# Performance work log

Measured on AMD Instinct MI355X. Metric: run time of the kernel, lower is better.

The kernel has to match this reference:

```python
import jax, jax.numpy as jnp
import numpy as np

B, S = 2, 2048
HID = 2048
NH = 16
QLR, KVLR = 1536, 512
DN, DR, DV = 128, 64, 128
QHD = DN + DR  # 192
SCALE = 1.0 / np.sqrt(QHD)
ROPE_BASE = 10000.0


def rope_cos_sin(seq_len, dim):
    inv_freq = 1.0 / (ROPE_BASE ** (jnp.arange(0, dim, 2, dtype=jnp.float32) / dim))
    freqs = jnp.arange(seq_len, dtype=jnp.float32)[:, None] * inv_freq[None, :]  # [S, dim/2]
    emb = jnp.concatenate([freqs, freqs], axis=-1)  # [S, dim]
    return jnp.cos(emb), jnp.sin(emb)


def rotate_half(x):
    h = x.shape[-1] // 2
    return jnp.concatenate([-x[..., h:], x[..., :h]], axis=-1)


def apply_rope(x, cos, sin):
    # x: [B, S, H, D]; cos/sin: [S, D] broadcast per position
    c = cos[None, :, None, :]
    s = sin[None, :, None, :]
    return x * c + rotate_half(x) * s


def setup_inputs() -> dict:
    key = jax.random.key(0)
    ks = jax.random.split(key, 10)
    w = lambda k, shape: (jax.random.normal(k, shape, dtype=jnp.float32) * 0.02)
    causal = jnp.tril(jnp.ones((S, S), dtype=bool))[None, None]  # [1,1,S,S]
    return {
        "hidden_states": jax.random.normal(ks[0], (B, S, HID), dtype=jnp.float32),
        "causal_mask": causal,
        "w_q_a": w(ks[1], (HID, QLR)),
        "w_q_nope": w(ks[2], (QLR, NH * DN)),
        "w_q_rope": w(ks[3], (QLR, NH * DR)),
        "w_kv_a": w(ks[4], (HID, KVLR)),
        "w_k_nope": w(ks[5], (KVLR, NH * DN)),
        "w_k_rope": w(ks[6], (KVLR, NH * DR)),
        "w_v": w(ks[7], (KVLR, NH * DV)),
        "w_o": w(ks[8], (NH * DV, HID)),
    }


def reference(hidden_states, causal_mask, w_q_a, w_q_nope, w_q_rope,
              w_kv_a, w_k_nope, w_k_rope, w_v, w_o):
    b, s, _ = hidden_states.shape
    # LoRA-A compression
    q_c = hidden_states @ w_q_a      # [B,S,QLR]
    kv_c = hidden_states @ w_kv_a    # [B,S,KVLR]
    # LoRA-B expansions (split NOPE / ROPE)
    q_nope = (q_c @ w_q_nope).reshape(b, s, NH, DN)
    q_rope = (q_c @ w_q_rope).reshape(b, s, NH, DR)
    k_nope = (kv_c @ w_k_nope).reshape(b, s, NH, DN)
    k_rope = (kv_c @ w_k_rope).reshape(b, s, NH, DR)
    v = (kv_c @ w_v).reshape(b, s, NH, DV)
    # RoPE on the rope slices only
    cos, sin = rope_cos_sin(s, DR)
    q_rope = apply_rope(q_rope, cos, sin)
    k_rope = apply_rope(k_rope, cos, sin)
    q = jnp.concatenate([q_nope, q_rope], axis=-1)  # [B,S,H,192]
    k = jnp.concatenate([k_nope, k_rope], axis=-1)
    # attention
    scores = jnp.einsum('bqhd,bkhd->bhqk', q, k) * SCALE
    mask_add = jnp.where(causal_mask, 0.0, -10000.0)
    attn = jax.nn.softmax(scores + mask_add, axis=-1)
    out = jnp.einsum('bhqk,bkhd->bqhd', attn, v).reshape(b, s, NH * DV)
    return out @ w_o  # [B,S,HID]
```

## Files before the change

kernel.cpp:

```cpp
#include <hip/hip_runtime.h>
#include <hip/hip_bf16.h>
#include <stdint.h>

typedef __hip_bfloat16 bf16;
typedef __attribute__((ext_vector_type(8))) short bf16x8;
typedef __attribute__((ext_vector_type(4))) float f32x4;

#define MFMA16(a,b,c) __builtin_amdgcn_mfma_f32_16x16x32_bf16((a),(b),(c),0,0,0)

#define BATCH 2
#define S_LEN 2048
#define HID_D 2048
#define NHEAD 16
#define QLR_D 1536
#define KVLR_D 512
#define DN_D 128
#define DR_D 64
#define DV_D 128
#define QKD 192
#define ATT_SCALE 0.07216878364870322f

__device__ __forceinline__ void async_load16(const bf16* g, bf16* l) {
    __builtin_amdgcn_global_load_lds((const __attribute__((address_space(1))) uint32_t*)g,
                                     (__attribute__((address_space(3))) uint32_t*)l,
                                     16, 0, 0);
}

__device__ __forceinline__ unsigned short f2bf_bits(float f) {
    bf16 h = __float2bfloat16(f);
    return *reinterpret_cast<unsigned short*>(&h);
}

template <int CTRL>
__device__ __forceinline__ float dpp_mov(float x) {
    return __builtin_bit_cast(float,
        __builtin_amdgcn_update_dpp(0, __builtin_bit_cast(int, x), CTRL, 0xF, 0xF, true));
}
__device__ __forceinline__ float row_max16(float x) {
    x = fmaxf(x, dpp_mov<0xB1>(x));
    x = fmaxf(x, dpp_mov<0x4E>(x));
    x = fmaxf(x, dpp_mov<0x124>(x));
    x = fmaxf(x, dpp_mov<0x128>(x));
    return x;
}
__device__ __forceinline__ float row_sum16(float x) {
    x += dpp_mov<0xB1>(x);
    x += dpp_mov<0x4E>(x);
    x += dpp_mov<0x124>(x);
    x += dpp_mov<0x128>(x);
    return x;
}

__global__ void convert_bf16_kernel(const float* __restrict__ in, bf16* __restrict__ out, int n) {
    int idx = blockIdx.x * blockDim.x + threadIdx.x;
    int i4 = idx * 4;
    if (i4 >= n) return;
    float4 v = *(const float4*)(in + i4);
    ushort4 o;
    o.x = f2bf_bits(v.x);
    o.y = f2bf_bits(v.y);
    o.z = f2bf_bits(v.z);
    o.w = f2bf_bits(v.w);
    *(ushort4*)(out + i4) = o;
}

__global__ void transpose_convert_kernel(const float* __restrict__ in, bf16* __restrict__ out,
                                         int K, int N) {
    __shared__ float tile[32][33];
    int tx = threadIdx.x;
    int ty = threadIdx.y;
    int n0 = blockIdx.x * 32, k0 = blockIdx.y * 32;
#pragma unroll
    for (int i = 0; i < 4; i++)
        tile[ty + i * 8][tx] = in[(size_t)(k0 + ty + i * 8) * N + n0 + tx];
    __syncthreads();
#pragma unroll
    for (int i = 0; i < 4; i++)
        out[(size_t)(n0 + ty + i * 8) * K + k0 + tx] = __float2bfloat16(tile[tx][ty + i * 8]);
}

template <int MODE>
__global__ __launch_bounds__(256, 2)
void gemm_bt_kernel(const bf16* __restrict__ A, const bf16* __restrict__ Bt,
                    void* __restrict__ C, void* __restrict__ C2,
                    int M, int N, int K, int lda) {
    __shared__ __align__(16) bf16 As[128 * 64];
    __shared__ __align__(16) bf16 Bs[128 * 64];
    const int tid = threadIdx.x;
    const int wave = tid >> 6, lane = tid & 63;
    const int quad = lane >> 4, l16 = lane & 15;
    const int wm = (wave >> 1) * 64, wn = (wave & 1) * 64;
    const int m0 = blockIdx.y * 128, n0 = blockIdx.x * 128;

    f32x4 acc[4][4];
#pragma unroll
    for (int i = 0; i < 4; i++)
#pragma unroll
        for (int j = 0; j < 4; j++)
            acc[i][j] = (f32x4){0.f, 0.f, 0.f, 0.f};

    const bf16* ga = A + (size_t)m0 * lda;
    const bf16* gb = Bt + (size_t)n0 * K;

    for (int k0 = 0; k0 < K; k0 += 64) {
        __syncthreads();
#pragma unroll
        for (int i = 0; i < 4; i++) {
            int chunk = i * 256 + tid;
            int row = chunk >> 3, cseg = chunk & 7;
            int wbase = i * 256 + wave * 64;
            async_load16(ga + (size_t)row * lda + k0 + cseg * 8, &As[wbase * 8]);
            async_load16(gb + (size_t)row * K + k0 + cseg * 8, &Bs[wbase * 8]);
        }
        __syncthreads();
#pragma unroll
        for (int kk = 0; kk < 64; kk += 32) {
            bf16x8 af[4], bfr[4];
#pragma unroll
            for (int t = 0; t < 4; t++) {
                af[t]  = *(const bf16x8*)&As[(wm + t * 16 + l16) * 64 + kk + quad * 8];
                bfr[t] = *(const bf16x8*)&Bs[(wn + t * 16 + l16) * 64 + kk + quad * 8];
            }
#pragma unroll
            for (int tm = 0; tm < 4; tm++)
#pragma unroll
                for (int tn = 0; tn < 4; tn++)
                    acc[tm][tn] = MFMA16(af[tm], bfr[tn], acc[tm][tn]);
        }
    }
#pragma unroll
    for (int tm = 0; tm < 4; tm++)
#pragma unroll
        for (int tn = 0; tn < 4; tn++) {
            const int col = n0 + wn + tn * 16 + l16;
            const int row0 = m0 + wm + tm * 16 + quad * 4;
            if constexpr (MODE == 4) {
                if (n0 >= 3072) {
                    ushort4 pk;
                    pk.x = f2bf_bits(acc[tm][tn][0]);
                    pk.y = f2bf_bits(acc[tm][tn][1]);
                    pk.z = f2bf_bits(acc[tm][tn][2]);
                    pk.w = f2bf_bits(acc[tm][tn][3]);
                    *(ushort4*)((bf16*)C2 + (size_t)(col - 3072) * M + row0) = pk;
                    continue;
                }
            }
#pragma unroll
            for (int r = 0; r < 4; r++) {
                const int row = row0 + r;
                const float v = acc[tm][tn][r];
                if constexpr (MODE == 0)
                    ((bf16*)C)[(size_t)row * N + col] = __float2bfloat16(v);
                else if constexpr (MODE == 1)
                    ((float*)C)[(size_t)row * N + col] = v;
                else if constexpr (MODE == 2) {
                    if (n0 < 2048) {
                        int hh = col >> 7, dd = col & 127;
                        ((bf16*)C)[(size_t)row * (NHEAD * QKD) + hh * QKD + dd] =
                            __float2bfloat16(v);
                    } else {
                        int c2 = col - 2048, hh = c2 >> 6, dd = c2 & 63;
                        ((bf16*)C)[(size_t)row * (NHEAD * QKD) + hh * QKD + 128 + dd] =
                            __float2bfloat16(v);
                    }
                } else {
                    if (n0 < 2048) {
                        int hh = col >> 7, dd = col & 127;
                        ((bf16*)C)[(size_t)row * (NHEAD * QKD) + hh * QKD + dd] =
                            __float2bfloat16(v);
                    } else {
                        int c2 = col - 2048, hh = c2 >> 6, dd = c2 & 63;
                        ((bf16*)C)[(size_t)row * (NHEAD * QKD) + hh * QKD + 128 + dd] =
                            __float2bfloat16(v);
                    }
                }
            }
        }
}

__global__ void rope_kernel(bf16* __restrict__ buf, int nrows) {
    int idx = blockIdx.x * blockDim.x + threadIdx.x;
    if (idx >= nrows * NHEAD * 32) return;
    int j = idx & 31;
    int h = (idx >> 5) & (NHEAD - 1);
    int row = idx >> 9;
    int pos = row & (S_LEN - 1);
    float inv = __expf(-(float)j * (9.210340371976184f / 32.f));
    float f = (float)pos * inv;
    float c = __cosf(f), s = __sinf(f);
    bf16* p = buf + (size_t)row * (NHEAD * QKD) + h * QKD + 128 + j;
    float x1 = __bfloat162float(p[0]);
    float x2 = __bfloat162float(p[32]);
    p[0]  = __float2bfloat16(x1 * c - x2 * s);
    p[32] = __float2bfloat16(x2 * c + x1 * s);
}

__global__ __launch_bounds__(256, 2)
void attn_kernel(const bf16* __restrict__ qf_g, const bf16* __restrict__ kf_g,
                 const bf16* __restrict__ vT, bf16* __restrict__ o_out) {
    __shared__ __align__(16) bf16 k_s[64 * QKD];
    __shared__ __align__(16) bf16 vt_s[128 * 64];
    __shared__ __align__(16) bf16 p_s[4 * 32 * 64];

    const int tid = threadIdx.x;
    const int wave = tid >> 6, lane = tid & 63;
    const int quad = lane >> 4, l16 = lane & 15;
    const int bh = blockIdx.y;
    const int qt = (bh < 16) ? (gridDim.x - 1 - blockIdx.x) : blockIdx.x;
    const int q0 = qt * 128;
    const int b = bh >> 4, h = bh & 15;
    const int tokbase = b * S_LEN;
    const int M = BATCH * S_LEN;

    const int wq = q0 + wave * 32;
    bf16x8 qfr[2][6];
#pragma unroll
    for (int mt = 0; mt < 2; mt++) {
        const bf16* qrow = qf_g + (size_t)(tokbase + wq + mt * 16 + l16) * (NHEAD * QKD)
                                + h * QKD + quad * 8;
#pragma unroll
        for (int kk = 0; kk < 6; kk++)
            qfr[mt][kk] = *(const bf16x8*)(qrow + kk * 32);
    }

    float m_run[2][4], l_run[2][4];
#pragma unroll
    for (int mt = 0; mt < 2; mt++)
#pragma unroll
        for (int r = 0; r < 4; r++) { m_run[mt][r] = -1e30f; l_run[mt][r] = 0.f; }
    f32x4 oacc[2][8];
#pragma unroll
    for (int mt = 0; mt < 2; mt++)
#pragma unroll
        for (int d = 0; d < 8; d++) oacc[mt][d] = (f32x4){0.f, 0.f, 0.f, 0.f};

    const int niter = q0 / 64 + 2;
    for (int it = 0; it < niter; it++) {
        const int kv0 = it * 64;
        __syncthreads();
#pragma unroll
        for (int i = 0; i < 6; i++) {
            int c = i * 256 + tid;
            int row = c / 24, seg = c % 24;
            async_load16(kf_g + (size_t)(tokbase + kv0 + row) * (NHEAD * QKD) + h * QKD + seg * 8,
                         &k_s[(i * 256 + wave * 64) * 8]);
        }
#pragma unroll
        for (int i = 0; i < 4; i++) {
            int c = i * 256 + tid;
            int d = c >> 3, seg = c & 7;
            async_load16(vT + (size_t)(h * 128 + d) * M + tokbase + kv0 + seg * 8,
                         &vt_s[(i * 256 + wave * 64) * 8]);
        }
        __syncthreads();

        if (kv0 <= wq + 31) {
            const bool do0 = kv0 <= wq + 15;
            f32x4 sa[2][4];
#pragma unroll
            for (int mt = 0; mt < 2; mt++)
#pragma unroll
                for (int nt = 0; nt < 4; nt++) sa[mt][nt] = (f32x4){0.f, 0.f, 0.f, 0.f};
#pragma unroll
            for (int kk = 0; kk < 6; kk++) {
                bf16x8 bk[4];
#pragma unroll
                for (int nt = 0; nt < 4; nt++)
                    bk[nt] = *(const bf16x8*)&k_s[(nt * 16 + l16) * QKD + kk * 32 + quad * 8];
#pragma unroll
                for (int mt = 0; mt < 2; mt++)
#pragma unroll
                    for (int nt = 0; nt < 4; nt++)
                        sa[mt][nt] = MFMA16(qfr[mt][kk], bk[nt], sa[mt][nt]);
            }

            auto softmax_mt = [&](int mt) {
                const int qmin = wq + mt * 16;
                const bool needMask = (kv0 + 63) > qmin;
                float alpha[4];
#pragma unroll
                for (int r = 0; r < 4; r++) {
                    const int qpos = qmin + quad * 4 + r;
                    float mx = m_run[mt][r];
                    float sv[4];
#pragma unroll
                    for (int nt = 0; nt < 4; nt++) {
                        float x = sa[mt][nt][r];
                        if (needMask && (kv0 + nt * 16 + l16 > qpos)) x = -1e30f;
                        sv[nt] = x;
                        mx = fmaxf(mx, x);
                    }
                    mx = row_max16(mx);
                    float rs = 0.f;
#pragma unroll
                    for (int nt = 0; nt < 4; nt++) {
                        float p = __expf(ATT_SCALE * (sv[nt] - mx));
                        sv[nt] = p;
                        rs += p;
                    }
                    rs = row_sum16(rs);
                    alpha[r] = __expf(ATT_SCALE * (m_run[mt][r] - mx));
                    l_run[mt][r] = alpha[r] * l_run[mt][r] + rs;
                    m_run[mt][r] = mx;
                    const int row = mt * 16 + quad * 4 + r;
#pragma unroll
                    for (int nt = 0; nt < 4; nt++)
                        p_s[wave * 2048 + row * 64 + ((nt ^ quad) << 4) + l16] =
                            __float2bfloat16(sv[nt]);
                }
#pragma unroll
                for (int d = 0; d < 8; d++)
#pragma unroll
                    for (int r = 0; r < 4; r++) oacc[mt][d][r] *= alpha[r];
            };
            if (do0) softmax_mt(0);
            softmax_mt(1);

#pragma unroll
            for (int kk = 0; kk < 2; kk++) {
                bf16x8 bv[8];
#pragma unroll
                for (int d = 0; d < 8; d++)
                    bv[d] = *(const bf16x8*)&vt_s[(d * 16 + l16) * 64 + kk * 32 + quad * 8];
                const int grp = (kk * 2 + (quad >> 1)) ^ (l16 >> 2);
                const int lo8 = (quad & 1) * 8;
                bf16x8 ap1 = *(const bf16x8*)&p_s[wave * 2048 + (16 + l16) * 64 + (grp << 4) + lo8];
                if (do0) {
                    bf16x8 ap0 = *(const bf16x8*)&p_s[wave * 2048 + l16 * 64 + (grp << 4) + lo8];
#pragma unroll
                    for (int d = 0; d < 8; d++) oacc[0][d] = MFMA16(ap0, bv[d], oacc[0][d]);
                }
#pragma unroll
                for (int d = 0; d < 8; d++) oacc[1][d] = MFMA16(ap1, bv[d], oacc[1][d]);
            }
        }
    }

#pragma unroll
    for (int mt = 0; mt < 2; mt++)
#pragma unroll
        for (int d = 0; d < 8; d++)
#pragma unroll
            for (int r = 0; r < 4; r++) {
                int qrow = wq + mt * 16 + quad * 4 + r;
                int col = h * DV_D + d * 16 + l16;
                o_out[(size_t)(tokbase + qrow) * (NHEAD * DV_D) + col] =
                    __float2bfloat16(oacc[mt][d][r] / l_run[mt][r]);
            }
}

extern "C" void kernel_launch(void* const* d_in, const int* in_sizes, int n_in,
                              void* d_out, int out_size, void* d_ws, size_t ws_size,
                              hipStream_t stream) {
    const float* hs        = (const float*)d_in[0];
    const float* w_q_a     = (const float*)d_in[2];
    const float* w_q_nope  = (const float*)d_in[3];
    const float* w_q_rope  = (const float*)d_in[4];
    const float* w_kv_a    = (const float*)d_in[5];
    const float* w_k_nope  = (const float*)d_in[6];
    const float* w_k_rope  = (const float*)d_in[7];
    const float* w_v       = (const float*)d_in[8];
    const float* w_o       = (const float*)d_in[9];
    float* out = (float*)d_out;

    const int M = BATCH * S_LEN;

    char* wsp = (char*)d_ws;
    auto alloc = [&](size_t elems) {
        bf16* p = (bf16*)wsp;
        wsp += ((elems * 2 + 255) / 256) * 256;
        return p;
    };
    bf16* hs_b     = alloc((size_t)M * HID_D);
    bf16* w_a_t    = alloc((size_t)2048 * HID_D);
    bf16* wq_up_t  = alloc((size_t)3072 * QLR_D);
    bf16* wkv_up_t = alloc((size_t)5120 * KVLR_D);
    bf16* wo_t     = alloc((size_t)HID_D * (NHEAD * DV_D));
    bf16* qkv_c    = alloc((size_t)M * 2048);
    bf16* q_full   = alloc((size_t)M * NHEAD * QKD);
    bf16* k_full   = alloc((size_t)M * NHEAD * QKD);
    bf16* vT       = alloc((size_t)NHEAD * DV_D * M);
    bf16* a_out    = alloc((size_t)M * NHEAD * DV_D);

    {
        int n = M * HID_D;
        convert_bf16_kernel<<<(n / 4 + 255) / 256, 256, 0, stream>>>(hs, hs_b, n);
    }
    dim3 tb(32, 8);
    transpose_convert_kernel<<<dim3(QLR_D / 32, HID_D / 32), tb, 0, stream>>>(w_q_a, w_a_t, HID_D, QLR_D);
    transpose_convert_kernel<<<dim3(KVLR_D / 32, HID_D / 32), tb, 0, stream>>>(w_kv_a, w_a_t + (size_t)QLR_D * HID_D, HID_D, KVLR_D);
    transpose_convert_kernel<<<dim3(2048 / 32, QLR_D / 32), tb, 0, stream>>>(w_q_nope, wq_up_t, QLR_D, 2048);
    transpose_convert_kernel<<<dim3(1024 / 32, QLR_D / 32), tb, 0, stream>>>(w_q_rope, wq_up_t + (size_t)2048 * QLR_D, QLR_D, 1024);
    transpose_convert_kernel<<<dim3(2048 / 32, KVLR_D / 32), tb, 0, stream>>>(w_k_nope, wkv_up_t, KVLR_D, 2048);
    transpose_convert_kernel<<<dim3(1024 / 32, KVLR_D / 32), tb, 0, stream>>>(w_k_rope, wkv_up_t + (size_t)2048 * KVLR_D, KVLR_D, 1024);
    transpose_convert_kernel<<<dim3(2048 / 32, KVLR_D / 32), tb, 0, stream>>>(w_v, wkv_up_t + (size_t)3072 * KVLR_D, KVLR_D, 2048);
    transpose_convert_kernel<<<dim3(HID_D / 32, 2048 / 32), tb, 0, stream>>>(w_o, wo_t, NHEAD * DV_D, HID_D);

    gemm_bt_kernel<0><<<dim3(2048 / 128, M / 128), 256, 0, stream>>>(hs_b, w_a_t, qkv_c, nullptr, M, 2048, HID_D, HID_D);
    gemm_bt_kernel<2><<<dim3(3072 / 128, M / 128), 256, 0, stream>>>(qkv_c, wq_up_t, q_full, nullptr, M, 3072, QLR_D, 2048);
    gemm_bt_kernel<4><<<dim3(5120 / 128, M / 128), 256, 0, stream>>>(qkv_c + QLR_D, wkv_up_t, k_full, vT, M, 5120, KVLR_D, 2048);

    {
        int n = M * NHEAD * 32;
        rope_kernel<<<(n + 255) / 256, 256, 0, stream>>>(q_full, M);
        rope_kernel<<<(n + 255) / 256, 256, 0, stream>>>(k_full, M);
    }

    attn_kernel<<<dim3(S_LEN / 128, BATCH * NHEAD), 256, 0, stream>>>(q_full, k_full, vT, a_out);

    gemm_bt_kernel<1><<<dim3(HID_D / 128, M / 128), 256, 0, stream>>>(a_out, wo_t, out, nullptr, M, HID_D, NHEAD * DV_D, NHEAD * DV_D);

    (void)in_sizes; (void)n_in; (void)out_size; (void)ws_size;
}
```

Measured before the change: 480.5 us.

## Split attention work across 8 waves with 16 query rows each

The attention kernel now launches 512 threads per block, and each of the 8 waves handles 16 query rows instead of 32. This halves the per-wave register state (Q fragments, accumulators, softmax stats) so more waves can be resident, and it spreads the cooperative K/V tile loads over more threads. In exchange, each wave reuses every K/V fragment loaded from LDS across only one 16-row tile, so LDS reads per FLOP roughly double. More waves also meet at each block barrier.

```diff
diff --git a/kernel.cpp b/kernel.cpp
--- a/kernel.cpp
+++ b/kernel.cpp
@@ -195,12 +195,12 @@
     p[32] = __float2bfloat16(x2 * c + x1 * s);
 }
 
-__global__ __launch_bounds__(256, 2)
+__global__ __launch_bounds__(512, 4)
 void attn_kernel(const bf16* __restrict__ qf_g, const bf16* __restrict__ kf_g,
                  const bf16* __restrict__ vT, bf16* __restrict__ o_out) {
     __shared__ __align__(16) bf16 k_s[64 * QKD];
     __shared__ __align__(16) bf16 vt_s[128 * 64];
-    __shared__ __align__(16) bf16 p_s[4 * 32 * 64];
+    __shared__ __align__(16) bf16 p_s[8 * 16 * 64];
 
     const int tid = threadIdx.x;
     const int wave = tid >> 6, lane = tid & 63;
@@ -212,141 +212,116 @@
     const int tokbase = b * S_LEN;
     const int M = BATCH * S_LEN;
 
-    const int wq = q0 + wave * 32;
-    bf16x8 qfr[2][6];
-#pragma unroll
-    for (int mt = 0; mt < 2; mt++) {
-        const bf16* qrow = qf_g + (size_t)(tokbase + wq + mt * 16 + l16) * (NHEAD * QKD)
+    const int wq = q0 + wave * 16;
+    bf16x8 qfr[6];
+    {
+        const bf16* qrow = qf_g + (size_t)(tokbase + wq + l16) * (NHEAD * QKD)
                                 + h * QKD + quad * 8;
 #pragma unroll
         for (int kk = 0; kk < 6; kk++)
-            qfr[mt][kk] = *(const bf16x8*)(qrow + kk * 32);
-    }
-
-    float m_run[2][4], l_run[2][4];
-#pragma unroll
-    for (int mt = 0; mt < 2; mt++)
-#pragma unroll
-        for (int r = 0; r < 4; r++) { m_run[mt][r] = -1e30f; l_run[mt][r] = 0.f; }
-    f32x4 oacc[2][8];
-#pragma unroll
-    for (int mt = 0; mt < 2; mt++)
-#pragma unroll
-        for (int d = 0; d < 8; d++) oacc[mt][d] = (f32x4){0.f, 0.f, 0.f, 0.f};
+            qfr[kk] = *(const bf16x8*)(qrow + kk * 32);
+    }
+
+    float m_run[4], l_run[4];
+#pragma unroll
+    for (int r = 0; r < 4; r++) { m_run[r] = -1e30f; l_run[r] = 0.f; }
+    f32x4 oacc[8];
+#pragma unroll
+    for (int d = 0; d < 8; d++) oacc[d] = (f32x4){0.f, 0.f, 0.f, 0.f};
 
     const int niter = q0 / 64 + 2;
     for (int it = 0; it < niter; it++) {
         const int kv0 = it * 64;
         __syncthreads();
 #pragma unroll
-        for (int i = 0; i < 6; i++) {
-            int c = i * 256 + tid;
+        for (int i = 0; i < 3; i++) {
+            int c = i * 512 + tid;
             int row = c / 24, seg = c % 24;
             async_load16(kf_g + (size_t)(tokbase + kv0 + row) * (NHEAD * QKD) + h * QKD + seg * 8,
-                         &k_s[(i * 256 + wave * 64) * 8]);
-        }
-#pragma unroll
-        for (int i = 0; i < 4; i++) {
-            int c = i * 256 + tid;
+                         &k_s[(i * 512 + wave * 64) * 8]);
+        }
+#pragma unroll
+        for (int i = 0; i < 2; i++) {
+            int c = i * 512 + tid;
             int d = c >> 3, seg = c & 7;
             async_load16(vT + (size_t)(h * 128 + d) * M + tokbase + kv0 + seg * 8,
-                         &vt_s[(i * 256 + wave * 64) * 8]);
+                         &vt_s[(i * 512 + wave * 64) * 8]);
         }
         __syncthreads();
 
-        if (kv0 <= wq + 31) {
-            const bool do0 = kv0 <= wq + 15;
-            f32x4 sa[2][4];
-#pragma unroll
-            for (int mt = 0; mt < 2; mt++)
-#pragma unroll
-                for (int nt = 0; nt < 4; nt++) sa[mt][nt] = (f32x4){0.f, 0.f, 0.f, 0.f};
+        if (kv0 <= wq + 15) {
+            f32x4 sa[4];
+#pragma unroll
+            for (int nt = 0; nt < 4; nt++) sa[nt] = (f32x4){0.f, 0.f, 0.f, 0.f};
 #pragma unroll
             for (int kk = 0; kk < 6; kk++) {
-                bf16x8 bk[4];
+#pragma unroll
+                for (int nt = 0; nt < 4; nt++) {
+                    bf16x8 bk = *(const bf16x8*)&k_s[(nt * 16 + l16) * QKD + kk * 32 + quad * 8];
+                    sa[nt] = MFMA16(qfr[kk], bk, sa[nt]);
+                }
+            }
+
+            const bool needMask = (kv0 + 63) > wq;
+            float alpha[4];
+#pragma unroll
+            for (int r = 0; r < 4; r++) {
+                const int qpos = wq + quad * 4 + r;
+                float mx = m_run[r];
+                float sv[4];
+#pragma unroll
+                for (int nt = 0; nt < 4; nt++) {
+                    float x = sa[nt][r];
+                    if (needMask && (kv0 + nt * 16 + l16 > qpos)) x = -1e30f;
+                    sv[nt] = x;
+                    mx = fmaxf(mx, x);
+                }
+                mx = row_max16(mx);
+                float rs = 0.f;
+#pragma unroll
+                for (int nt = 0; nt < 4; nt++) {
+                    float p = __expf(ATT_SCALE * (sv[nt] - mx));
+                    sv[nt] = p;
+                    rs += p;
+                }
+                rs = row_sum16(rs);
+                alpha[r] = __expf(ATT_SCALE * (m_run[r] - mx));
+                l_run[r] = alpha[r] * l_run[r] + rs;
+                m_run[r] = mx;
+                const int row = quad * 4 + r;
 #pragma unroll
                 for (int nt = 0; nt < 4; nt++)
-                    bk[nt] = *(const bf16x8*)&k_s[(nt * 16 + l16) * QKD + kk * 32 + quad * 8];
-#pragma unroll
-                for (int mt = 0; mt < 2; mt++)
-#pragma unroll
-                    for (int nt = 0; nt < 4; nt++)
-                        sa[mt][nt] = MFMA16(qfr[mt][kk], bk[nt], sa[mt][nt]);
-            }
-
-            auto softmax_mt = [&](int mt) {
-                const int qmin = wq + mt * 16;
-                const bool needMask = (kv0 + 63) > qmin;
-                float alpha[4];
-#pragma unroll
-                for (int r = 0; r < 4; r++) {
-                    const int qpos = qmin + quad * 4 + r;
-                    float mx = m_run[mt][r];
-                    float sv[4];
-#pragma unroll
-                    for (int nt = 0; nt < 4; nt++) {
-                        float x = sa[mt][nt][r];
-                        if (needMask && (kv0 + nt * 16 + l16 > qpos)) x = -1e30f;
-                        sv[nt] = x;
-                        mx = fmaxf(mx, x);
-                    }
-                    mx = row_max16(mx);
-                    float rs = 0.f;
-#pragma unroll
-                    for (int nt = 0; nt < 4; nt++) {
-                        float p = __expf(ATT_SCALE * (sv[nt] - mx));
-                        sv[nt] = p;
-                        rs += p;
-                    }
-                    rs = row_sum16(rs);
-                    alpha[r] = __expf(ATT_SCALE * (m_run[mt][r] - mx));
-                    l_run[mt][r] = alpha[r] * l_run[mt][r] + rs;
-                    m_run[mt][r] = mx;
-                    const int row = mt * 16 + quad * 4 + r;
-#pragma unroll
-                    for (int nt = 0; nt < 4; nt++)
-                        p_s[wave * 2048 + row * 64 + ((nt ^ quad) << 4) + l16] =
-                            __float2bfloat16(sv[nt]);
-                }
-#pragma unroll
-                for (int d = 0; d < 8; d++)
-#pragma unroll
-                    for (int r = 0; r < 4; r++) oacc[mt][d][r] *= alpha[r];
-            };
-            if (do0) softmax_mt(0);
-            softmax_mt(1);
+                    p_s[wave * 1024 + row * 64 + ((nt ^ quad) << 4) + l16] =
+                        __float2bfloat16(sv[nt]);
+            }
+#pragma unroll
+            for (int d = 0; d < 8; d++)
+#pragma unroll
+                for (int r = 0; r < 4; r++) oacc[d][r] *= alpha[r];
 
 #pragma unroll
             for (int kk = 0; kk < 2; kk++) {
-                bf16x8 bv[8];
-#pragma unroll
-                for (int d = 0; d < 8; d++)
-                    bv[d] = *(const bf16x8*)&vt_s[(d * 16 + l16) * 64 + kk * 32 + quad * 8];
                 const int grp = (kk * 2 + (quad >> 1)) ^ (l16 >> 2);
                 const int lo8 = (quad & 1) * 8;
-                bf16x8 ap1 = *(const bf16x8*)&p_s[wave * 2048 + (16 + l16) * 64 + (grp << 4) + lo8];
-                if (do0) {
-                    bf16x8 ap0 = *(const bf16x8*)&p_s[wave * 2048 + l16 * 64 + (grp << 4) + lo8];
-#pragma unroll
-                    for (int d = 0; d < 8; d++) oacc[0][d] = MFMA16(ap0, bv[d], oacc[0][d]);
-                }
-#pragma unroll
-                for (int d = 0; d < 8; d++) oacc[1][d] = MFMA16(ap1, bv[d], oacc[1][d]);
-            }
-        }
-    }
-
-#pragma unroll
-    for (int mt = 0; mt < 2; mt++)
-#pragma unroll
-        for (int d = 0; d < 8; d++)
-#pragma unroll
-            for (int r = 0; r < 4; r++) {
-                int qrow = wq + mt * 16 + quad * 4 + r;
-                int col = h * DV_D + d * 16 + l16;
-                o_out[(size_t)(tokbase + qrow) * (NHEAD * DV_D) + col] =
-                    __float2bfloat16(oacc[mt][d][r] / l_run[mt][r]);
-            }
+                bf16x8 ap = *(const bf16x8*)&p_s[wave * 1024 + l16 * 64 + (grp << 4) + lo8];
+#pragma unroll
+                for (int d = 0; d < 8; d++) {
+                    bf16x8 bv = *(const bf16x8*)&vt_s[(d * 16 + l16) * 64 + kk * 32 + quad * 8];
+                    oacc[d] = MFMA16(ap, bv, oacc[d]);
+                }
+            }
+        }
+    }
+
+#pragma unroll
+    for (int d = 0; d < 8; d++)
+#pragma unroll
+        for (int r = 0; r < 4; r++) {
+            int qrow = wq + quad * 4 + r;
+            int col = h * DV_D + d * 16 + l16;
+            o_out[(size_t)(tokbase + qrow) * (NHEAD * DV_D) + col] =
+                __float2bfloat16(oacc[d][r] / l_run[r]);
+        }
 }
 
 extern "C" void kernel_launch(void* const* d_in, const int* in_sizes, int n_in,
@@ -406,7 +381,7 @@
         rope_kernel<<<(n + 255) / 256, 256, 0, stream>>>(k_full, M);
     }
 
-    attn_kernel<<<dim3(S_LEN / 128, BATCH * NHEAD), 256, 0, stream>>>(q_full, k_full, vT, a_out);
+    attn_kernel<<<dim3(S_LEN / 128, BATCH * NHEAD), 512, 0, stream>>>(q_full, k_full, vT, a_out);
 
     gemm_bt_kernel<1><<<dim3(HID_D / 128, M / 128), 256, 0, stream>>>(a_out, wo_t, out, nullptr, M, HID_D, NHEAD * DV_D, NHEAD * DV_D);
 
```

Result: slower. 491.2 us (+2.2%).
